# Performance work log

Measured on AMD Instinct MI355X. Metric: run time of the kernel, lower is better.

Reference implementation:

```python
import jax, jax.numpy as jnp
import numpy as np

D_MODEL = 768
N_HEADS = 12
HEAD_DIM = D_MODEL // N_HEADS
FFN_DIM = 3072
MAX_WAVELENGTH = 10000.0
ROPE_PERCENT = 0.5
NORM_EPS = 1e-5


def setup_inputs() -> dict:
    key = jax.random.key(0)
    ks = jax.random.split(key, 12)
    B, C, S = 2, 16, 128
    init = lambda k, shape: (jax.random.normal(k, shape, dtype=jnp.float32) * 0.02)
    return {
        "hidden_state": jax.random.normal(ks[0], (B, C, S, D_MODEL), dtype=jnp.float32),
        "wq": init(ks[1], (D_MODEL, D_MODEL)), "bq": jnp.zeros((D_MODEL,), jnp.float32),
        "wk": init(ks[2], (D_MODEL, D_MODEL)), "bk": jnp.zeros((D_MODEL,), jnp.float32),
        "wv": init(ks[3], (D_MODEL, D_MODEL)), "bv": jnp.zeros((D_MODEL,), jnp.float32),
        "wo": init(ks[4], (D_MODEL, D_MODEL)), "bo": jnp.zeros((D_MODEL,), jnp.float32),
        "attn_biases": init(ks[5], (N_HEADS, 2)),
        "ln1_g": jnp.ones((D_MODEL,), jnp.float32), "ln1_b": jnp.zeros((D_MODEL,), jnp.float32),
        "ln3_g": jnp.ones((D_MODEL,), jnp.float32), "ln3_b": jnp.zeros((D_MODEL,), jnp.float32),
        "w1": init(ks[6], (D_MODEL, FFN_DIM)), "b1": jnp.zeros((FFN_DIM,), jnp.float32),
        "w2": init(ks[7], (FFN_DIM, D_MODEL)), "b2": jnp.zeros((D_MODEL,), jnp.float32),
    }


def _layernorm(x, g, b):
    mu = jnp.mean(x, axis=-1, keepdims=True)
    var = jnp.mean(jnp.square(x - mu), axis=-1, keepdims=True)
    return (x - mu) * jax.lax.rsqrt(var + NORM_EPS) * g + b


def _apply_p_rope(x, positions):
    # x: [B, H, T, head_dim]; p-RoPE: only rope_percent of frequency bands rotate.
    half = HEAD_DIM // 2
    rope_angles = int(ROPE_PERCENT * HEAD_DIM) // 2  # 16
    fraction = 2.0 * jnp.arange(rope_angles, dtype=jnp.float32) / HEAD_DIM
    timescale = jnp.concatenate([
        MAX_WAVELENGTH ** fraction,
        jnp.full((half - rope_angles,), jnp.inf, dtype=jnp.float32),
    ])  # [half]
    angles = positions[:, None].astype(jnp.float32) / timescale[None, :]  # [T, half]
    sin = jnp.sin(angles)[None, None]  # [1,1,T,half]
    cos = jnp.cos(angles)[None, None]
    x1, x2 = jnp.split(x, 2, axis=-1)
    return jnp.concatenate([x1 * cos - x2 * sin, x2 * cos + x1 * sin], axis=-1)


def _forward(hidden_state, wq, bq, wk, bk, wv, bv, wo, bo, attn_biases,
             ln1_g, ln1_b, ln3_g, ln3_b, w1, b1, w2, b2):
    B, C, S, D = hidden_state.shape
    T = C * S
    flat = hidden_state.reshape(B, T, D)

    # --- attention sublayer (pre-norm) ---
    ni = _layernorm(flat, ln1_g, ln1_b)
    scaling = HEAD_DIM ** -0.5
    q = (ni @ wq + bq) * scaling
    k = ni @ wk + bk
    v = ni @ wv + bv
    to_heads = lambda t: t.reshape(B, T, N_HEADS, HEAD_DIM).transpose(0, 2, 1, 3)
    q, k, v = to_heads(q), to_heads(k), to_heads(v)  # [B,H,T,hd]

    positions = jnp.arange(T)
    k = _apply_p_rope(k, positions)
    q = _apply_p_rope(q, positions)

    scores = jnp.einsum("bhtd,bhsd->bhts", q, k)  # [B,H,T,T]
    variate_ids = positions // S
    same = (variate_ids[:, None] == variate_ids[None, :]).astype(scores.dtype)  # [T,T]
    variate_bias = (same[None, :, :] * attn_biases[:, 0][:, None, None]
                    + (1.0 - same[None, :, :]) * attn_biases[:, 1][:, None, None])  # [H,T,T]
    scores = scores + variate_bias[None]
    probs = jax.nn.softmax(scores, axis=-1)
    attn = jnp.einsum("bhts,bhsd->bhtd", probs, v)
    attn = attn.transpose(0, 2, 1, 3).reshape(B, T, D)
    attn = attn @ wo + bo

    flat = flat + attn  # residual (pre-norm -> no post-norm here)

    # --- feed-forward sublayer (pre-norm) ---
    ff_in = _layernorm(flat, ln3_g, ln3_b)
    ff = jax.nn.gelu(ff_in @ w1 + b1, approximate=False) @ w2 + b2
    flat = flat + ff

    return flat.reshape(B, C, S, D)


def reference(hidden_state, wq, bq, wk, bk, wv, bv, wo, bo, attn_biases,
              ln1_g, ln1_b, ln3_g, ln3_b, w1, b1, w2, b2):
    return _forward(hidden_state, wq, bq, wk, bk, wv, bv, wo, bo, attn_biases,
                    ln1_g, ln1_b, ln3_g, ln3_b, w1, b1, w2, b2)
```

## Files before the change

### kernel.cpp

```cpp
#include <hip/hip_runtime.h>
#include <cmath>


typedef __bf16 bf16_t;
typedef bf16_t bf16x8 __attribute__((ext_vector_type(8)));
typedef float floatx4 __attribute__((ext_vector_type(4)));
typedef unsigned int u32x4 __attribute__((ext_vector_type(4)));

#define MFMA(a, b, c) __builtin_amdgcn_mfma_f32_16x16x32_bf16((a), (b), (c), 0, 0, 0)
#define LOG2E 1.44269504088896340736f

__device__ __forceinline__ bf16_t f2bf(float f) { return (bf16_t)f; }

__device__ __forceinline__ float fexp2(float x) {
  return __builtin_amdgcn_exp2f(x);
}

__device__ __forceinline__ void g2l16(const void* g, void* l) {
  __builtin_amdgcn_global_load_lds(
      (const __attribute__((address_space(1))) unsigned int*)g,
      (__attribute__((address_space(3))) unsigned int*)l, 16, 0, 0);
}

__device__ __forceinline__ void wait_vm4() {
  asm volatile("s_waitcnt vmcnt(4)" ::: "memory");
}
__device__ __forceinline__ void wait_vm0() {
  asm volatile("s_waitcnt vmcnt(0)" ::: "memory");
}

__device__ __forceinline__ unsigned cvt_pk_bf16(float lo, float hi) {
  unsigned r;
  asm("v_cvt_pk_bf16_f32 %0, %1, %2" : "=v"(r) : "v"(lo), "v"(hi));
  return r;
}
__device__ __forceinline__ void pl32swap(unsigned& a, unsigned& b) {
  asm("v_permlane32_swap_b32 %0, %1" : "+v"(a), "+v"(b));
}
__device__ __forceinline__ void pl16swap(unsigned& a, unsigned& b) {
  asm("v_permlane16_swap_b32 %0, %1" : "+v"(a), "+v"(b));
}

struct PrepP {
  const float *wq, *wk, *wv, *wo, *w1, *w2;
  bf16_t *wqkvT, *woT, *w1T, *w2T;
  const float *hs, *g1, *be1;
  bf16_t* ni;
};

__global__ __launch_bounds__(256) void k_prep(PrepP p) {
  __shared__ float shm[32 * 33];
  const int bid = blockIdx.x;
  if (bid < 6912) {
    const float* in;
    bf16_t* out;
    int R, C, tx, ty;
    if (bid < 2304) {
      int m = bid / 576, lo = bid % 576;
      in = (m == 0) ? p.wq : (m == 1) ? p.wk : (m == 2) ? p.wv : p.wo;
      out = (m < 3) ? p.wqkvT + (size_t)m * 768 * 768 : p.woT;
      R = 768; C = 768; tx = lo % 24; ty = lo / 24;
    } else if (bid < 4608) {
      int lo = bid - 2304;
      in = p.w1; out = p.w1T; R = 768; C = 3072; tx = lo % 96; ty = lo / 96;
    } else {
      int lo = bid - 4608;
      in = p.w2; out = p.w2T; R = 3072; C = 768; tx = lo % 24; ty = lo / 24;
    }
    const int c0 = tx * 32, r0 = ty * 32;
    const int lx = threadIdx.x & 31, ly = threadIdx.x >> 5;
#pragma unroll
    for (int p4 = 0; p4 < 4; p4++) {
      int r = ly + p4 * 8;
      shm[r * 33 + lx] = in[(size_t)(r0 + r) * C + c0 + lx];
    }
    __syncthreads();
#pragma unroll
    for (int p4 = 0; p4 < 4; p4++) {
      int r = ly + p4 * 8;
      out[(size_t)(c0 + r) * R + r0 + lx] = f2bf(shm[lx * 33 + r]);
    }
  } else {
    const int row = bid - 6912;
    const float* xr = p.hs + (size_t)row * 768;
    const int t = threadIdx.x;
    float v0 = xr[t], v1 = xr[t + 256], v2 = xr[t + 512];
    float s = v0 + v1 + v2;
    float s2 = v0 * v0 + v1 * v1 + v2 * v2;
#pragma unroll
    for (int off = 32; off; off >>= 1) {
      s += __shfl_xor(s, off);
      s2 += __shfl_xor(s2, off);
    }
    const int w = t >> 6;
    if ((t & 63) == 0) { shm[w] = s; shm[4 + w] = s2; }
    __syncthreads();
    s = shm[0] + shm[1] + shm[2] + shm[3];
    s2 = shm[4] + shm[5] + shm[6] + shm[7];
    const float mu = s * (1.0f / 768.0f);
    const float var = s2 * (1.0f / 768.0f) - mu * mu;
    const float rstd = rsqrtf(var + 1e-5f);
    bf16_t* orow = p.ni + (size_t)row * 768;
    orow[t]       = f2bf((v0 - mu) * rstd * p.g1[t]       + p.be1[t]);
    orow[t + 256] = f2bf((v1 - mu) * rstd * p.g1[t + 256] + p.be1[t + 256]);
    orow[t + 512] = f2bf((v2 - mu) * rstd * p.g1[t + 512] + p.be1[t + 512]);
  }
}

__global__ __launch_bounds__(256) void k_layernorm(
    const float* __restrict__ x, const float* __restrict__ g,
    const float* __restrict__ b, bf16_t* __restrict__ out) {
  const int row = blockIdx.x;
  const float* xr = x + (size_t)row * 768;
  const int t = threadIdx.x;
  float v0 = xr[t], v1 = xr[t + 256], v2 = xr[t + 512];
  float s = v0 + v1 + v2;
  float s2 = v0 * v0 + v1 * v1 + v2 * v2;
#pragma unroll
  for (int off = 32; off; off >>= 1) {
    s += __shfl_xor(s, off);
    s2 += __shfl_xor(s2, off);
  }
  __shared__ float ra[4], rb[4];
  const int w = t >> 6;
  if ((t & 63) == 0) { ra[w] = s; rb[w] = s2; }
  __syncthreads();
  s = ra[0] + ra[1] + ra[2] + ra[3];
  s2 = rb[0] + rb[1] + rb[2] + rb[3];
  const float mu = s * (1.0f / 768.0f);
  const float var = s2 * (1.0f / 768.0f) - mu * mu;
  const float rstd = rsqrtf(var + 1e-5f);
  bf16_t* orow = out + (size_t)row * 768;
  orow[t]       = f2bf((v0 - mu) * rstd * g[t]       + b[t]);
  orow[t + 256] = f2bf((v1 - mu) * rstd * g[t + 256] + b[t + 256]);
  orow[t + 512] = f2bf((v2 - mu) * rstd * g[t + 512] + b[t + 512]);
}

struct GemmP {
  const bf16_t* A;
  const bf16_t* Bt;
  int M, N, K, mode;
  const float* bias0;
  const float* bias1;
  const float* bias2;
  float* outF;
  bf16_t* outB0;
  bf16_t* outB1;
  bf16_t* outB2;
};

__global__ __launch_bounds__(256, 3) void k_gemm(GemmP p) {
  __shared__ bf16_t lds[18432];
  const int tid = threadIdx.x;
  const int lane = tid & 63, wave = tid >> 6;
  const int quad = lane >> 4, l15 = lane & 15;
  const int wm = (wave >> 1) * 64, wn = (wave & 1) * 64;
  const int m0 = blockIdx.y * 128, n0 = blockIdx.x * 128;

  const char* gA[4];
  const char* gB[4];
#pragma unroll
  for (int pp = 0; pp < 4; pp++) {
    int slot = wave * 256 + pp * 64 + lane;
    int r = slot >> 3;
    int c8 = ((slot & 7) ^ (r & 7)) << 3;
    gA[pp] = (const char*)(p.A + (size_t)(m0 + r) * p.K + c8);
    gB[pp] = (const char*)(p.Bt + (size_t)(n0 + r) * p.K + c8);
  }

  int offA[4], offB[4];
#pragma unroll
  for (int i = 0; i < 4; i++) {
    int ra = wm + i * 16 + l15;
    offA[i] = ra * 64 + ((quad * 8) ^ ((ra & 7) << 3));
    int rb = wn + i * 16 + l15;
    offB[i] = rb * 64 + ((quad * 8) ^ ((rb & 7) << 3));
  }

  const floatx4 z4 = {0.f, 0.f, 0.f, 0.f};
  floatx4 acc[4][4];
#pragma unroll
  for (int i = 0; i < 4; i++)
#pragma unroll
    for (int j = 0; j < 4; j++) acc[i][j] = z4;

  const int KT = p.K >> 6;
  bf16_t* Ad = lds + wave * 2048;
  bf16_t* Bd = lds + 8192 + wave * 2048;

  for (int kt = 0; kt < KT; kt++) {
    const size_t kb = (size_t)kt * 128;
#pragma unroll
    for (int pp = 0; pp < 4; pp++) {
      g2l16(gA[pp] + kb, Ad + pp * 512);
      g2l16(gB[pp] + kb, Bd + pp * 512);
    }
    __syncthreads();
#pragma unroll
    for (int ks = 0; ks < 2; ks++) {
      bf16x8 af[4], bfr[4];
#pragma unroll
      for (int i = 0; i < 4; i++) {
        af[i] = *(const bf16x8*)(lds + (offA[i] ^ (ks * 32)));
        bfr[i] = *(const bf16x8*)(lds + 8192 + (offB[i] ^ (ks * 32)));
      }
#pragma unroll
      for (int i = 0; i < 4; i++)
#pragma unroll
        for (int j = 0; j < 4; j++) acc[i][j] = MFMA(af[i], bfr[j], acc[i][j]);
    }
    __syncthreads();
  }

  char* scr = (char*)lds + wave * 9216;

  if (p.mode == 0) {
    const int gnw = n0 + wn;
    const int region = gnw / 768;
    const int rem = gnw - region * 768;
    const int h = rem >> 6;
    const int b = (m0 + wm) >> 11;
    const int t0 = (m0 + wm) & 2047;
    const float* bias = (region == 0) ? p.bias0 : (region == 1 ? p.bias1 : p.bias2);
    float bb[4];
#pragma unroll
    for (int j = 0; j < 4; j++) bb[j] = bias[h * 64 + j * 16 + l15];
    bf16_t* sb = (bf16_t*)scr;
    if (region < 2) {
      const float scale = (region == 0) ? 0.125f * LOG2E : 1.0f;
      const float inv_ts = exp2f(-(float)l15 * (13.287712379549449f / 32.0f));
#pragma unroll
      for (int i = 0; i < 4; i++) {
#pragma unroll
        for (int reg = 0; reg < 4; reg++) {
          int tl = i * 16 + quad * 4 + reg;
          float sn, cs;
          __sincosf((float)(t0 + tl) * inv_ts, &sn, &cs);
          float v0 = (acc[i][0][reg] + bb[0]) * scale;
          float v1 = (acc[i][1][reg] + bb[1]) * scale;
          float v2 = (acc[i][2][reg] + bb[2]) * scale;
          float v3 = (acc[i][3][reg] + bb[3]) * scale;
          sb[tl * 72 + l15]      = f2bf(v0 * cs - v2 * sn);
          sb[tl * 72 + 16 + l15] = f2bf(v1);
          sb[tl * 72 + 32 + l15] = f2bf(v2 * cs + v0 * sn);
          sb[tl * 72 + 48 + l15] = f2bf(v3);
        }
      }
      __syncthreads();
      bf16_t* outp = (region == 0) ? p.outB0 : p.outB1;
      bf16_t* ob = outp + (((size_t)(b * 12 + h) * 2048 + t0) << 6);
#pragma unroll
      for (int pp = 0; pp < 8; pp++) {
        int row = pp * 8 + (lane >> 3), ch = (lane & 7) << 3;
        *(bf16x8*)(ob + row * 64 + ch) = *(const bf16x8*)&sb[row * 72 + ch];
      }
    } else {
#pragma unroll
      for (int i = 0; i < 4; i++)
#pragma unroll
        for (int j = 0; j < 4; j++)
#pragma unroll
          for (int reg = 0; reg < 4; reg++)
            sb[(j * 16 + l15) * 72 + i * 16 + quad * 4 + reg] =
                f2bf(acc[i][j][reg] + bb[j]);
      __syncthreads();
      bf16_t* ob = p.outB2 + (((size_t)(b * 12 + h)) << 17) + t0;
#pragma unroll
      for (int pp = 0; pp < 8; pp++) {
        int d = pp * 8 + (lane >> 3), ch = (lane & 7) << 3;
        *(bf16x8*)(ob + (size_t)d * 2048 + ch) = *(const bf16x8*)&sb[d * 72 + ch];
      }
    }
  } else {
    bf16_t* sb = (bf16_t*)scr;
    float bb[4];
#pragma unroll
    for (int j = 0; j < 4; j++) bb[j] = p.bias0[n0 + wn + j * 16 + l15];
#pragma unroll
    for (int i = 0; i < 4; i++)
#pragma unroll
      for (int j = 0; j < 4; j++)
#pragma unroll
        for (int reg = 0; reg < 4; reg++) {
          int tl = i * 16 + quad * 4 + reg;
          float x = acc[i][j][reg] + bb[j];
          float gv = 0.5f * x * (1.0f + erff(x * 0.70710678118654752f));
          sb[tl * 72 + j * 16 + l15] = f2bf(gv);
        }
    __syncthreads();
#pragma unroll
    for (int pp = 0; pp < 8; pp++) {
      int row = pp * 8 + (lane >> 3), ch = (lane & 7) << 3;
      *(bf16x8*)(p.outB0 + (size_t)(m0 + wm + row) * p.N + n0 + wn + ch) =
          *(const bf16x8*)&sb[row * 72 + ch];
    }
  }
}

__global__ __launch_bounds__(256, 4) void k_gemm64(
    const bf16_t* __restrict__ A, const bf16_t* __restrict__ Bt, int N, int K,
    const float* __restrict__ bias, const float* __restrict__ resid,
    float* __restrict__ outF) {
  __shared__ bf16_t lds[16384];
  const int tid = threadIdx.x;
  const int lane = tid & 63, wave = tid >> 6;
  const int quad = lane >> 4, l15 = lane & 15;
  const int wm = (wave >> 1) * 32, wn = (wave & 1) * 32;
  const int m0 = blockIdx.y * 64, n0 = blockIdx.x * 64;

  const char* gA[4];
  const char* gB[4];
#pragma unroll
  for (int pp = 0; pp < 4; pp++) {
    int slot = wave * 256 + pp * 64 + lane;
    int r = slot >> 4;
    int c = ((slot & 15) ^ (r & 7)) << 3;
    gA[pp] = (const char*)(A + (size_t)(m0 + r) * K + c);
    gB[pp] = (const char*)(Bt + (size_t)(n0 + r) * K + c);
  }

  const floatx4 z4 = {0.f, 0.f, 0.f, 0.f};
  floatx4 acc[2][2];
#pragma unroll
  for (int i = 0; i < 2; i++)
#pragma unroll
    for (int j = 0; j < 2; j++) acc[i][j] = z4;

  const int KT = K >> 7;
  bf16_t* Ad = lds + wave * 2048;
  bf16_t* Bd = lds + 8192 + wave * 2048;

  for (int kt = 0; kt < KT; kt++) {
    const size_t kb = (size_t)kt * 256;
#pragma unroll
    for (int pp = 0; pp < 4; pp++) {
      g2l16(gA[pp] + kb, Ad + pp * 512);
      g2l16(gB[pp] + kb, Bd + pp * 512);
    }
    __syncthreads();
#pragma unroll
    for (int ks = 0; ks < 4; ks++) {
      bf16x8 af[2], bfr[2];
#pragma unroll
      for (int i = 0; i < 2; i++) {
        int ra = wm + i * 16 + l15;
        af[i] = *(const bf16x8*)(lds + ra * 128 +
                                 (((ks * 4 + quad) ^ (ra & 7)) << 3));
        int rb = wn + i * 16 + l15;
        bfr[i] = *(const bf16x8*)(lds + 8192 + rb * 128 +
                                  (((ks * 4 + quad) ^ (rb & 7)) << 3));
      }
#pragma unroll
      for (int i = 0; i < 2; i++)
#pragma unroll
        for (int j = 0; j < 2; j++) acc[i][j] = MFMA(af[i], bfr[j], acc[i][j]);
    }
    __syncthreads();
  }

  float* s4 = (float*)lds + wave * 1024;
#pragma unroll
  for (int i = 0; i < 2; i++)
#pragma unroll
    for (int j = 0; j < 2; j++)
#pragma unroll
      for (int reg = 0; reg < 4; reg++)
        s4[(i * 16 + quad * 4 + reg) * 32 + j * 16 + l15] = acc[i][j][reg];
  __syncthreads();
#pragma unroll
  for (int pp = 0; pp < 4; pp++) {
    int row = pp * 8 + (lane >> 3);
    int c4 = (lane & 7) * 4;
    floatx4 v = *(const floatx4*)&s4[row * 32 + c4];
    size_t goff = (size_t)(m0 + wm + row) * N + n0 + wn + c4;
    floatx4 rv = *(const floatx4*)(resid + goff);
    floatx4 bv = *(const floatx4*)(bias + n0 + wn + c4);
    *(floatx4*)(outF + goff) = v + rv + bv;
  }
}

__global__ __launch_bounds__(256, 3) void k_flash(
    const bf16_t* __restrict__ qh, const bf16_t* __restrict__ kh,
    const bf16_t* __restrict__ vt, const float* __restrict__ ab,
    bf16_t* __restrict__ attnA) {
  __shared__ bf16_t sm[25088];

  const int tid = threadIdx.x, lane = tid & 63, wave = tid >> 6;
  const int quad = lane >> 4, l15 = lane & 15;
  const int qtile = blockIdx.x, bh = blockIdx.y;
  const int h = bh % 12, bq = bh / 12;
  const int myv = qtile >> 1;

  bf16_t* wb = sm + wave * 6144;
  bf16_t* Kb0 = wb;
  bf16_t* Vs = wb + 2048;

  const bf16_t* Qg = qh + ((size_t)bh * 2048 + qtile * 64) * 64;
  const bf16_t* Kg = kh + ((size_t)bh * 2048 + wave * 16) * 64;

  const char* gK[2];
#pragma unroll
  for (int i = 0; i < 2; i++) {
    int sl = i * 8 + (lane >> 3);
    int cs = (lane & 7) ^ (sl & 7);
    gK[i] = (const char*)(Kg + sl * 64 + cs * 8);
  }
  const char* gV[2];
#pragma unroll
  for (int i = 0; i < 2; i++) {
    int d = i * 32 + (lane >> 1);
    int hs = (lane & 1) ^ ((d >> 2) & 1);
    gV[i] = (const char*)(vt + ((size_t)(bh * 64 + d)) * 2048 + wave * 16 + hs * 8);
  }

  bf16x8 qf[4][2];
#pragma unroll
  for (int mt = 0; mt < 4; mt++)
#pragma unroll
    for (int ks = 0; ks < 2; ks++)
      qf[mt][ks] = *(const bf16x8*)(Qg + (size_t)(mt * 16 + l15) * 64 +
                                    ks * 32 + quad * 8);

  int offKr[2];
#pragma unroll
  for (int ks = 0; ks < 2; ks++)
    offKr[ks] = l15 * 64 + ((((ks << 2) + quad) ^ (l15 & 7)) << 3);
  int offV[4];
#pragma unroll
  for (int nt = 0; nt < 4; nt++) {
    int d = nt * 16 + l15;
    offV[nt] = (quad >> 1) * 1024 + d * 16 +
               (((quad & 1) ^ ((d >> 2) & 1)) << 3);
  }

  const floatx4 z4 = {0.f, 0.f, 0.f, 0.f};
  floatx4 oacc[4][4];
  float l_mt[4];
  unsigned pA[4], pB[4];
#pragma unroll
  for (int mt = 0; mt < 4; mt++)
#pragma unroll
    for (int nt = 0; nt < 4; nt++) oacc[mt][nt] = z4;
#pragma unroll
  for (int mt = 0; mt < 4; mt++) l_mt[mt] = 0.f;

  const float bc_same = ab[h * 2] * LOG2E;
  const float bc_diff = ab[h * 2 + 1] * LOG2E;
  const float ratio = fexp2(bc_same - bc_diff);
  const floatx4 bD4 = {bc_diff, bc_diff, bc_diff, bc_diff};

  g2l16(gK[0], Kb0);
  g2l16(gK[1], Kb0 + 512);
  g2l16(gV[0], Vs);
  g2l16(gV[1], Vs + 512);

#pragma unroll 2
  for (int kv = 0; kv < 32; kv++) {
    const int nkv = (kv + 1) & 31;
    {
      const size_t kbK = (size_t)nkv * 8192, kbV = (size_t)nkv * 128;
      bf16_t* Kd = Kb0 + (nkv & 1) * 1024;
      bf16_t* Vd = Vs + ((((nkv >> 1) & 1) << 1) + (nkv & 1)) * 1024;
      g2l16(gK[0] + kbK, Kd);
      g2l16(gK[1] + kbK, Kd + 512);
      g2l16(gV[0] + kbV, Vd);
      g2l16(gV[1] + kbV, Vd + 512);
    }
    wait_vm4();

    const bf16_t* Kc = Kb0 + (kv & 1) * 1024;
    floatx4 sacc[4];
    {
      const bf16x8 kf0 = *(const bf16x8*)(Kc + offKr[0]);
      const bf16x8 kf1 = *(const bf16x8*)(Kc + offKr[1]);
#pragma unroll
      for (int mt = 0; mt < 4; mt++) {
        sacc[mt] = MFMA(kf0, qf[mt][0], bD4);
        sacc[mt] = MFMA(kf1, qf[mt][1], sacc[mt]);
      }
    }

    float pr[4][4];
    if ((kv >> 1) == myv) {
#pragma unroll
      for (int mt = 0; mt < 4; mt++)
#pragma unroll
        for (int r = 0; r < 4; r++) pr[mt][r] = fexp2(sacc[mt][r]) * ratio;
    } else {
#pragma unroll
      for (int mt = 0; mt < 4; mt++)
#pragma unroll
        for (int r = 0; r < 4; r++) pr[mt][r] = fexp2(sacc[mt][r]);
    }

    if (!(kv & 1)) {
#pragma unroll
      for (int mt = 0; mt < 4; mt++) {
        l_mt[mt] += (pr[mt][0] + pr[mt][1]) + (pr[mt][2] + pr[mt][3]);
        pA[mt] = cvt_pk_bf16(pr[mt][0], pr[mt][1]);
        pB[mt] = cvt_pk_bf16(pr[mt][2], pr[mt][3]);
      }
    } else {
      bf16x8 vf[4];
      const int vb = ((kv >> 1) & 1) * 2048;
#pragma unroll
      for (int nt = 0; nt < 4; nt++)
        vf[nt] = *(const bf16x8*)(Vs + vb + offV[nt]);
#pragma unroll
      for (int mt = 0; mt < 4; mt++) {
        l_mt[mt] += (pr[mt][0] + pr[mt][1]) + (pr[mt][2] + pr[mt][3]);
        unsigned b0 = cvt_pk_bf16(pr[mt][0], pr[mt][1]);
        unsigned b1 = cvt_pk_bf16(pr[mt][2], pr[mt][3]);
        unsigned a0 = pA[mt], a1 = pB[mt];
        pl32swap(a0, b0);
        pl16swap(a0, b0);
        pl32swap(a1, b1);
        pl16swap(a1, b1);
        u32x4 w;
        w[0] = a0; w[1] = a1; w[2] = b0; w[3] = b1;
        const bf16x8 pf = __builtin_bit_cast(bf16x8, w);
#pragma unroll
        for (int nt = 0; nt < 4; nt++)
          oacc[mt][nt] = MFMA(pf, vf[nt], oacc[mt][nt]);
      }
    }
  }

  wait_vm0();

#pragma unroll
  for (int mt = 0; mt < 4; mt++) {
    float v = l_mt[mt];
    v += __shfl_xor(v, 16);
    v += __shfl_xor(v, 32);
    l_mt[mt] = v;
  }
  float* lred = (float*)(sm + 24576);
  if (quad == 0) {
#pragma unroll
    for (int mt = 0; mt < 4; mt++)
      lred[wave * 64 + mt * 16 + l15] = l_mt[mt];
  }
#pragma unroll
  for (int mt = 0; mt < 4; mt++)
#pragma unroll
    for (int nt = 0; nt < 4; nt++)
#pragma unroll
      for (int reg = 0; reg < 4; reg++)
        wb[(mt * 16 + quad * 4 + reg) * 64 + nt * 16 + l15] =
            f2bf(oacc[mt][nt][reg]);
  __syncthreads();

  const int q = tid >> 2, dg = (tid & 3) * 16;
  const float inv =
      1.0f / (lred[q] + lred[64 + q] + lred[128 + q] + lred[192 + q]);
  float o[16];
#pragma unroll
  for (int j = 0; j < 16; j++) o[j] = 0.f;
#pragma unroll
  for (int w = 0; w < 4; w++) {
    const bf16x8 a = *(const bf16x8*)(sm + w * 6144 + q * 64 + dg);
    const bf16x8 b = *(const bf16x8*)(sm + w * 6144 + q * 64 + dg + 8);
#pragma unroll
    for (int j = 0; j < 8; j++) {
      o[j] += (float)a[j];
      o[8 + j] += (float)b[j];
    }
  }
  bf16x8 r0, r1;
#pragma unroll
  for (int j = 0; j < 8; j++) {
    r0[j] = f2bf(o[j] * inv);
    r1[j] = f2bf(o[8 + j] * inv);
  }
  bf16_t* outp =
      attnA + ((size_t)(bq * 2048 + qtile * 64 + q)) * 768 + h * 64 + dg;
  *(bf16x8*)outp = r0;
  *(bf16x8*)(outp + 8) = r1;
}

extern "C" void kernel_launch(void* const* d_in, const int* in_sizes, int n_in,
                              void* d_out, int out_size, void* d_ws,
                              size_t ws_size, hipStream_t stream) {
  const float* hs  = (const float*)d_in[0];
  const float* wq  = (const float*)d_in[1];
  const float* bq  = (const float*)d_in[2];
  const float* wk  = (const float*)d_in[3];
  const float* bk  = (const float*)d_in[4];
  const float* wv  = (const float*)d_in[5];
  const float* bv  = (const float*)d_in[6];
  const float* wo  = (const float*)d_in[7];
  const float* bo  = (const float*)d_in[8];
  const float* ab  = (const float*)d_in[9];
  const float* g1  = (const float*)d_in[10];
  const float* be1 = (const float*)d_in[11];
  const float* g3  = (const float*)d_in[12];
  const float* be3 = (const float*)d_in[13];
  const float* w1  = (const float*)d_in[14];
  const float* b1  = (const float*)d_in[15];
  const float* w2  = (const float*)d_in[16];
  const float* b2  = (const float*)d_in[17];

  char* ws = (char*)d_ws;
  size_t off = 0;
  auto alloc = [&](size_t bytes) -> void* {
    void* p = ws + off;
    off += (bytes + 255) & ~(size_t)255;
    return p;
  };
  bf16_t* wqkvT = (bf16_t*)alloc((size_t)2304 * 768 * 2);
  bf16_t* woT   = (bf16_t*)alloc((size_t)768 * 768 * 2);
  bf16_t* w1T   = (bf16_t*)alloc((size_t)3072 * 768 * 2);
  bf16_t* w2T   = (bf16_t*)alloc((size_t)768 * 3072 * 2);
  bf16_t* ni    = (bf16_t*)alloc((size_t)4096 * 768 * 2);
  bf16_t* qhB   = (bf16_t*)alloc((size_t)24 * 2048 * 64 * 2);
  bf16_t* khB   = (bf16_t*)alloc((size_t)24 * 2048 * 64 * 2);
  bf16_t* vtB   = (bf16_t*)alloc((size_t)24 * 64 * 2048 * 2);
  bf16_t* attnA = (bf16_t*)alloc((size_t)4096 * 768 * 2);
  float*  resid1 = (float*)alloc((size_t)4096 * 768 * 4);
  bf16_t* ffn1o = qhB;

  PrepP pp = {wq, wk, wv, wo, w1, w2, wqkvT, woT, w1T, w2T, hs, g1, be1, ni};
  k_prep<<<11008, 256, 0, stream>>>(pp);

  GemmP gqkv = {ni, wqkvT, 4096, 2304, 768, 0,
                bq, bk, bv, nullptr, qhB, khB, vtB};
  k_gemm<<<dim3(18, 32), 256, 0, stream>>>(gqkv);

  k_flash<<<dim3(32, 24), 256, 0, stream>>>(qhB, khB, vtB, ab, attnA);

  k_gemm64<<<dim3(12, 64), 256, 0, stream>>>(attnA, woT, 768, 768, bo, hs,
                                             resid1);

  k_layernorm<<<4096, 256, 0, stream>>>(resid1, g3, be3, ni);

  GemmP gf1 = {ni, w1T, 4096, 3072, 768, 2,
               b1, nullptr, nullptr, nullptr, ffn1o, nullptr, nullptr};
  k_gemm<<<dim3(24, 32), 256, 0, stream>>>(gf1);

  k_gemm64<<<dim3(12, 64), 256, 0, stream>>>(ffn1o, w2T, 768, 3072, b2,
                                             resid1, (float*)d_out);
}
```

Baseline: 280.4 us.

## Triple-buffer K/V in flash kernel with two-step K prefetch

Reorganizes the per-wave LDS staging in the flash attention kernel into a three-slot rotating ring for K and V. K tiles are now prefetched two iterations ahead and V one ahead, and the wait count is relaxed from vmcnt(4) to vmcnt(6) so more loads stay in flight. The exp/ratio scaling is also folded into each branch, using a conditional multiply in place of the separate duplicated loops. The aim is to hide global-to-LDS latency better. In exchange the slot-index logic is more complex and V reads pick between slots per quad, which adds register pressure at 3 blocks per CU.

```diff
diff --git a/kernel.cpp b/kernel.cpp
--- a/kernel.cpp
+++ b/kernel.cpp
@@ -22,8 +22,8 @@
       (__attribute__((address_space(3))) unsigned int*)l, 16, 0, 0);
 }
 
-__device__ __forceinline__ void wait_vm4() {
-  asm volatile("s_waitcnt vmcnt(4)" ::: "memory");
+__device__ __forceinline__ void wait_vm6() {
+  asm volatile("s_waitcnt vmcnt(6)" ::: "memory");
 }
 __device__ __forceinline__ void wait_vm0() {
   asm volatile("s_waitcnt vmcnt(0)" ::: "memory");
@@ -392,8 +392,7 @@
   const int myv = qtile >> 1;
 
   bf16_t* wb = sm + wave * 6144;
-  bf16_t* Kb0 = wb;
-  bf16_t* Vs = wb + 2048;
+  bf16_t* Vb = wb + 3072;
 
   const bf16_t* Qg = qh + ((size_t)bh * 2048 + qtile * 64) * 64;
   const bf16_t* Kg = kh + ((size_t)bh * 2048 + wave * 16) * 64;
@@ -429,8 +428,7 @@
 #pragma unroll
   for (int nt = 0; nt < 4; nt++) {
     int d = nt * 16 + l15;
-    offV[nt] = (quad >> 1) * 1024 + d * 16 +
-               (((quad & 1) ^ ((d >> 2) & 1)) << 3);
+    offV[nt] = d * 16 + (((quad & 1) ^ ((d >> 2) & 1)) << 3);
   }
 
   const floatx4 z4 = {0.f, 0.f, 0.f, 0.f};
@@ -449,26 +447,28 @@
   const float ratio = fexp2(bc_same - bc_diff);
   const floatx4 bD4 = {bc_diff, bc_diff, bc_diff, bc_diff};
 
-  g2l16(gK[0], Kb0);
-  g2l16(gK[1], Kb0 + 512);
-  g2l16(gV[0], Vs);
-  g2l16(gV[1], Vs + 512);
+  g2l16(gK[0], wb);
+  g2l16(gK[1], wb + 512);
+  g2l16(gV[0], Vb);
+  g2l16(gV[1], Vb + 512);
+  g2l16(gK[0] + 8192, wb + 1024);
+  g2l16(gK[1] + 8192, wb + 1024 + 512);
+
+  int sa = 0, sb = 1, sc = 2;
 
 #pragma unroll 2
   for (int kv = 0; kv < 32; kv++) {
-    const int nkv = (kv + 1) & 31;
     {
-      const size_t kbK = (size_t)nkv * 8192, kbV = (size_t)nkv * 128;
-      bf16_t* Kd = Kb0 + (nkv & 1) * 1024;
-      bf16_t* Vd = Vs + ((((nkv >> 1) & 1) << 1) + (nkv & 1)) * 1024;
-      g2l16(gK[0] + kbK, Kd);
-      g2l16(gK[1] + kbK, Kd + 512);
-      g2l16(gV[0] + kbV, Vd);
-      g2l16(gV[1] + kbV, Vd + 512);
-    }
-    wait_vm4();
-
-    const bf16_t* Kc = Kb0 + (kv & 1) * 1024;
+      const size_t kbV = (size_t)((kv + 1) & 31) * 128;
+      g2l16(gV[0] + kbV, Vb + sb * 1024);
+      g2l16(gV[1] + kbV, Vb + sb * 1024 + 512);
+      const size_t kbK = (size_t)((kv + 2) & 31) * 8192;
+      g2l16(gK[0] + kbK, wb + sc * 1024);
+      g2l16(gK[1] + kbK, wb + sc * 1024 + 512);
+    }
+    wait_vm6();
+
+    const bf16_t* Kc = wb + sa * 1024;
     floatx4 sacc[4];
     {
       const bf16x8 kf0 = *(const bf16x8*)(Kc + offKr[0]);
@@ -479,51 +479,46 @@
         sacc[mt] = MFMA(kf1, qf[mt][1], sacc[mt]);
       }
     }
-
-    float pr[4][4];
-    if ((kv >> 1) == myv) {
-#pragma unroll
-      for (int mt = 0; mt < 4; mt++)
-#pragma unroll
-        for (int r = 0; r < 4; r++) pr[mt][r] = fexp2(sacc[mt][r]) * ratio;
+    const bool same = ((kv >> 1) == myv);
+
+    if (!(kv & 1)) {
+#pragma unroll
+      for (int mt = 0; mt < 4; mt++) {
+        float p0 = fexp2(sacc[mt][0]), p1 = fexp2(sacc[mt][1]);
+        float p2 = fexp2(sacc[mt][2]), p3 = fexp2(sacc[mt][3]);
+        if (same) { p0 *= ratio; p1 *= ratio; p2 *= ratio; p3 *= ratio; }
+        l_mt[mt] += (p0 + p1) + (p2 + p3);
+        pA[mt] = cvt_pk_bf16(p0, p1);
+        pB[mt] = cvt_pk_bf16(p2, p3);
+      }
     } else {
-#pragma unroll
-      for (int mt = 0; mt < 4; mt++)
-#pragma unroll
-        for (int r = 0; r < 4; r++) pr[mt][r] = fexp2(sacc[mt][r]);
-    }
-
-    if (!(kv & 1)) {
+      const int vbase = ((quad >> 1) ? sa : sc) * 1024;
+      bf16x8 vf[4];
+#pragma unroll
+      for (int nt = 0; nt < 4; nt++)
+        vf[nt] = *(const bf16x8*)(Vb + vbase + offV[nt]);
 #pragma unroll
       for (int mt = 0; mt < 4; mt++) {
-        l_mt[mt] += (pr[mt][0] + pr[mt][1]) + (pr[mt][2] + pr[mt][3]);
-        pA[mt] = cvt_pk_bf16(pr[mt][0], pr[mt][1]);
-        pB[mt] = cvt_pk_bf16(pr[mt][2], pr[mt][3]);
-      }
-    } else {
-      bf16x8 vf[4];
-      const int vb = ((kv >> 1) & 1) * 2048;
-#pragma unroll
-      for (int nt = 0; nt < 4; nt++)
-        vf[nt] = *(const bf16x8*)(Vs + vb + offV[nt]);
-#pragma unroll
-      for (int mt = 0; mt < 4; mt++) {
-        l_mt[mt] += (pr[mt][0] + pr[mt][1]) + (pr[mt][2] + pr[mt][3]);
-        unsigned b0 = cvt_pk_bf16(pr[mt][0], pr[mt][1]);
-        unsigned b1 = cvt_pk_bf16(pr[mt][2], pr[mt][3]);
+        float p0 = fexp2(sacc[mt][0]), p1 = fexp2(sacc[mt][1]);
+        float p2 = fexp2(sacc[mt][2]), p3 = fexp2(sacc[mt][3]);
+        if (same) { p0 *= ratio; p1 *= ratio; p2 *= ratio; p3 *= ratio; }
+        l_mt[mt] += (p0 + p1) + (p2 + p3);
+        unsigned b0 = cvt_pk_bf16(p0, p1);
+        unsigned b1 = cvt_pk_bf16(p2, p3);
         unsigned a0 = pA[mt], a1 = pB[mt];
         pl32swap(a0, b0);
         pl16swap(a0, b0);
         pl32swap(a1, b1);
         pl16swap(a1, b1);
-        u32x4 w;
-        w[0] = a0; w[1] = a1; w[2] = b0; w[3] = b1;
-        const bf16x8 pf = __builtin_bit_cast(bf16x8, w);
+        u32x4 wr;
+        wr[0] = a0; wr[1] = a1; wr[2] = b0; wr[3] = b1;
+        const bf16x8 pf = __builtin_bit_cast(bf16x8, wr);
 #pragma unroll
         for (int nt = 0; nt < 4; nt++)
           oacc[mt][nt] = MFMA(pf, vf[nt], oacc[mt][nt]);
       }
     }
+    int tmp = sa; sa = sb; sb = sc; sc = tmp;
   }
 
   wait_vm0();
```

Measured after the change: 264.4 us. 1.06x faster.
